# Kernel optimization log

Hardware: AMD Instinct MI355X
Metric: run time of the kernel (lower is better)

Reference implementation:

```python
import jax, jax.numpy as jnp
import numpy as np
import math

N, DIN, H, D = 3072, 512, 16, 64
HD = H * D


def mish(x):
    return x * jnp.tanh(jax.nn.softplus(x))


def setup_inputs() -> dict:
    key = jax.random.key(0)
    ks = jax.random.split(key, 10)
    s_in = 1.0 / math.sqrt(DIN)
    s_hd = 1.0 / math.sqrt(HD)
    return {
        "q": jax.random.normal(ks[0], (N, DIN), jnp.float32),
        "k": jax.random.normal(ks[1], (N, DIN), jnp.float32),
        "v": jax.random.normal(ks[2], (N, DIN), jnp.float32),
        "bias": jax.random.normal(ks[3], (N, N), jnp.float32),
        "mask": jax.random.randint(ks[4], (N, N), 0, 2, jnp.int32),
        # q/k/v projections (xavier-like init, zero bias as in _reset_parameters)
        "Wq": jax.random.normal(ks[5], (HD, DIN), jnp.float32) * s_in,
        "bq": jnp.zeros((HD,), jnp.float32),
        "Wk": jax.random.normal(ks[6], (HD, DIN), jnp.float32) * s_in,
        "bk": jnp.zeros((HD,), jnp.float32),
        "Wv": jax.random.normal(ks[7], (HD, DIN), jnp.float32) * s_in,
        "bv": jnp.zeros((HD,), jnp.float32),
        # o_proj = Linear(HD,HD) -> Mish -> Linear(HD,DIN)
        "Wo1": jax.random.normal(ks[8], (HD, HD), jnp.float32) * s_hd,
        "bo1": jnp.zeros((HD,), jnp.float32),
        "Wo2": jax.random.normal(ks[9], (DIN, HD), jnp.float32) * s_hd,
        "bo2": jnp.zeros((DIN,), jnp.float32),
    }


def reference(q, k, v, bias, mask, Wq, bq, Wk, bk, Wv, bv, Wo1, bo1, Wo2, bo2):
    # forward(..., embed_bias=True, embed_value=True) path
    n = q.shape[0]
    # project and split heads: [N, DIN] -> [H, N, D]
    qh = (q @ Wq.T + bq).reshape(n, H, D).transpose(1, 0, 2)
    kh = (k @ Wk.T + bk).reshape(n, H, D).transpose(1, 0, 2)
    vh = (v @ Wv.T + bv).reshape(n, H, D).transpose(1, 0, 2)
    # scaled dot product with additive bias (broadcast over heads) + mask fill
    logits = jnp.einsum('hnd,hmd->hnm', qh, kh) / math.sqrt(D)
    logits = logits + bias[None, :, :]
    logits = jnp.where(mask[None, :, :] == 0, jnp.float32(-9e15), logits)
    attn = jax.nn.softmax(logits, axis=-1)           # [H, N, N]
    vals = jnp.einsum('hnm,hmd->hnd', attn, vh)      # [H, N, D]
    vals = vals.transpose(1, 0, 2).reshape(n, HD)    # [N, H*D]
    # o_proj MLP (dropout = 0)
    out = mish(vals @ Wo1.T + bo1) @ Wo2.T + bo2     # [N, DIN]
    return (out, bias)
```

## Files before the change

kernel.cpp:

```cpp
#include <hip/hip_runtime.h>
#include <hip/hip_bf16.h>

#define NT 3072
#define DIN_ 512
#define NH 16
#define DH 64
#define HDIM 1024

typedef unsigned short u16;
typedef unsigned int u32;
typedef short short8 __attribute__((ext_vector_type(8)));
typedef float f32x4 __attribute__((ext_vector_type(4)));
typedef __bf16 bf16x8 __attribute__((ext_vector_type(8)));

__device__ __forceinline__ u16 f2bf(float f){
  union { float f; unsigned u; } v; v.f = f;
  unsigned r = v.u + 0x7fffu + ((v.u >> 16) & 1u);
  return (u16)(r >> 16);
}
__device__ __forceinline__ float bf2f(u16 b){
  union { unsigned u; float f; } v; v.u = ((unsigned)b) << 16;
  return v.f;
}

__global__ __launch_bounds__(256) void prep_k(
    const float* __restrict__ bias, const int* __restrict__ mask,
    u16* __restrict__ bm, float* __restrict__ bias_out)
{
  int i = blockIdx.x * 256 + threadIdx.x;
  f32x4 b = ((const f32x4*)bias)[i];
  int4 m = ((const int4*)mask)[i];
  ((f32x4*)bias_out)[i] = b;
  const int mm[4] = {m.x, m.y, m.z, m.w};
  union { u16 s[4]; unsigned long long ll; } pk;
  #pragma unroll
  for (int j = 0; j < 4; ++j)
    pk.s[j] = mm[j] ? f2bf(b[j]) : f2bf(-1e30f);
  ((unsigned long long*)bm)[i] = pk.ll;
}

__global__ __launch_bounds__(256) void cvtw_k(
    const float* __restrict__ Wq, const float* __restrict__ Wk,
    const float* __restrict__ Wv, const float* __restrict__ Wo1,
    const float* __restrict__ Wo2,
    u16* __restrict__ wqb, u16* __restrict__ wkb, u16* __restrict__ wvb,
    u16* __restrict__ wo1b, u16* __restrict__ wo2b)
{
  const float* src; u16* dst; int n4;
  switch (blockIdx.y) {
    case 0: src = Wq;  dst = wqb;  n4 = HDIM*DIN_/4; break;
    case 1: src = Wk;  dst = wkb;  n4 = HDIM*DIN_/4; break;
    case 2: src = Wv;  dst = wvb;  n4 = HDIM*DIN_/4; break;
    case 3: src = Wo1; dst = wo1b; n4 = HDIM*HDIM/4; break;
    default: src = Wo2; dst = wo2b; n4 = DIN_*HDIM/4; break;
  }
  int i = blockIdx.x * 256 + threadIdx.x;
  if (i >= n4) return;
  f32x4 v = ((const f32x4*)src)[i];
  ushort4 o;
  o.x = f2bf(v[0]); o.y = f2bf(v[1]); o.z = f2bf(v[2]); o.w = f2bf(v[3]);
  ((ushort4*)dst)[i] = o;
}

template<int A_BF16, int EPI>
__device__ __forceinline__ void gemm_body(
    const void* __restrict__ Aptr, const u16* __restrict__ W,
    const float* __restrict__ bvec, void* __restrict__ Cptr,
    int Nc, int K, float scale, int bm0, int bn0,
    u16* As, u16* Bs)
{
  const int tid = threadIdx.x;
  const int lane = tid & 63;
  const int wid = tid >> 6;
  const int wr = wid >> 1, wc = wid & 1;
  const int g = lane >> 4, lr = lane & 15;

  f32x4 acc[4][4] = {};

  for (int k0 = 0; k0 < K; k0 += 32) {
    __syncthreads();
    if (A_BF16) {
      const u16* A = (const u16*)Aptr;
      #pragma unroll
      for (int it = 0; it < 2; ++it) {
        int e = it*2048 + tid*8;
        int r = e >> 5, kk = e & 31;
        *(short8*)&As[r*40 + kk] = *(const short8*)&A[(size_t)(bm0+r)*K + k0 + kk];
      }
    } else {
      const float* A = (const float*)Aptr;
      #pragma unroll
      for (int it = 0; it < 4; ++it) {
        int e = it*1024 + tid*4;
        int r = e >> 5, kk = e & 31;
        f32x4 v = *(const f32x4*)&A[(size_t)(bm0+r)*K + k0 + kk];
        union { u16 s[4]; unsigned long long ll; } pk;
        #pragma unroll
        for (int jj = 0; jj < 4; ++jj) pk.s[jj] = f2bf(v[jj]);
        *(unsigned long long*)&As[r*40 + kk] = pk.ll;
      }
    }
    {
      #pragma unroll
      for (int it = 0; it < 2; ++it) {
        int e = it*2048 + tid*8;
        int r = e >> 5, kk = e & 31;
        *(short8*)&Bs[r*40 + kk] = *(const short8*)&W[(size_t)(bn0+r)*K + k0 + kk];
      }
    }
    __syncthreads();
    bf16x8 af[4], bfr[4];
    #pragma unroll
    for (int m = 0; m < 4; ++m)
      af[m] = *(const bf16x8*)&As[(wr*64 + m*16 + lr)*40 + g*8];
    #pragma unroll
    for (int n = 0; n < 4; ++n)
      bfr[n] = *(const bf16x8*)&Bs[(wc*64 + n*16 + lr)*40 + g*8];
    #pragma unroll
    for (int m = 0; m < 4; ++m)
      #pragma unroll
      for (int n = 0; n < 4; ++n)
        acc[m][n] = __builtin_amdgcn_mfma_f32_16x16x32_bf16(af[m], bfr[n], acc[m][n], 0, 0, 0);
  }

  #pragma unroll
  for (int m = 0; m < 4; ++m) {
    const int row0 = bm0 + wr*64 + m*16 + g*4;
    #pragma unroll
    for (int n = 0; n < 4; ++n) {
      const int col = bn0 + wc*64 + n*16 + lr;
      const float bb = bvec[col];
      #pragma unroll
      for (int j = 0; j < 4; ++j) {
        float x = acc[m][n][j] + bb;
        if (EPI == 0) x *= scale;
        if (EPI == 1) {
          float sp = (x > 15.f) ? x : log1pf(__expf(x));
          x = x * tanhf(sp);
        }
        if (EPI == 2)
          ((float*)Cptr)[(size_t)(row0+j)*Nc + col] = x;
        else
          ((u16*)Cptr)[(size_t)(row0+j)*Nc + col] = f2bf(x);
      }
    }
  }
}

template<int A_BF16, int EPI>
__global__ __launch_bounds__(256) void gemm_k(
    const void* __restrict__ Aptr, const u16* __restrict__ W,
    const float* __restrict__ bvec, void* __restrict__ Cptr,
    int Nc, int K, float scale)
{
  __shared__ __align__(16) u16 As[128*40];
  __shared__ __align__(16) u16 Bs[128*40];
  gemm_body<A_BF16, EPI>(Aptr, W, bvec, Cptr, Nc, K, scale,
                         blockIdx.x*128, blockIdx.y*128, As, Bs);
}

__global__ __launch_bounds__(256) void qkv_k(
    const float* __restrict__ q, const float* __restrict__ k,
    const float* __restrict__ v,
    const u16* __restrict__ wqb, const float* __restrict__ bq,
    const u16* __restrict__ wkb, const float* __restrict__ bk,
    const u16* __restrict__ wvb, const float* __restrict__ bv,
    u16* __restrict__ qh, u16* __restrict__ kh, u16* __restrict__ vh)
{
  __shared__ __align__(16) u16 As[128*40];
  __shared__ __align__(16) u16 Bs[128*40];
  const int sel = blockIdx.y >> 3;
  const float* A    = sel == 0 ? q   : (sel == 1 ? k   : v);
  const u16* W      = sel == 0 ? wqb : (sel == 1 ? wkb : wvb);
  const float* bvec = sel == 0 ? bq  : (sel == 1 ? bk  : bv);
  u16* C            = sel == 0 ? qh  : (sel == 1 ? kh  : vh);
  const float scale = sel == 0 ? 0.125f : 1.0f;
  gemm_body<0, 0>(A, W, bvec, C, HDIM, DIN_, scale,
                  blockIdx.x*128, (blockIdx.y & 7)*128, As, Bs);
}

__global__ __launch_bounds__(256) void attn_k(
    const u16* __restrict__ qh, const u16* __restrict__ kh,
    const u16* __restrict__ vh, const u16* __restrict__ bm,
    u16* __restrict__ vals)
{
  __shared__ __align__(16) u16 Qs[64*72];
  __shared__ __align__(16) u16 Ks[64*72];
  __shared__ __align__(16) u16 Vts[64*72];
  __shared__ __align__(16) u16 Ps[4][16*72];

  const int tid = threadIdx.x;
  const int lane = tid & 63;
  const int w = tid >> 6;
  const int g = lane >> 4, lr = lane & 15;
  const int i0 = blockIdx.x * 64;
  const int hoff = blockIdx.y * DH;

  #pragma unroll
  for (int it = 0; it < 2; ++it) {
    int c = it*256 + tid;
    int r = c >> 3, co = (c & 7) * 8;
    *(short8*)&Qs[r*72 + co] = *(const short8*)&qh[(size_t)(i0 + r)*HDIM + hoff + co];
  }
  __syncthreads();
  bf16x8 qf[2];
  #pragma unroll
  for (int kc = 0; kc < 2; ++kc)
    qf[kc] = *(const bf16x8*)&Qs[(w*16 + lr)*72 + kc*32 + g*8];

  f32x4 Oa[4] = {};
  float mr = -1e30f, ls = 0.f;
  const size_t bmrow = (size_t)(i0 + w*16 + lr) * NT;

  for (int j = 0; j < NT/64; ++j) {
    const int c0 = j * 64;
    __syncthreads();
    #pragma unroll
    for (int it = 0; it < 2; ++it) {
      int c = it*256 + tid;
      int r = c >> 3, co = (c & 7) * 8;
      *(short8*)&Ks[r*72 + co] = *(const short8*)&kh[(size_t)(c0 + r)*HDIM + hoff + co];
    }
    #pragma unroll
    for (int it = 0; it < 2; ++it) {
      int c = it*256 + tid;
      int vr = c >> 3, dco = (c & 7) * 8;
      short8 vv = *(const short8*)&vh[(size_t)(c0 + vr)*HDIM + hoff + dco];
      #pragma unroll
      for (int jj = 0; jj < 8; ++jj) {
        int d = dco + jj;
        int byte = d*144 + vr*2;
        byte ^= ((d >> 3) & 7) << 4;
        *(u16*)((char*)Vts + byte) = (u16)vv[jj];
      }
    }
    __syncthreads();

    f32x4 Sa[4];
    #pragma unroll
    for (int n = 0; n < 4; ++n) {
      ushort4 bb = *(const ushort4*)&bm[bmrow + c0 + n*16 + g*4];
      Sa[n][0] = bf2f(bb.x); Sa[n][1] = bf2f(bb.y);
      Sa[n][2] = bf2f(bb.z); Sa[n][3] = bf2f(bb.w);
    }
    #pragma unroll
    for (int kc = 0; kc < 2; ++kc)
      #pragma unroll
      for (int n = 0; n < 4; ++n) {
        bf16x8 kb = *(const bf16x8*)&Ks[(n*16 + lr)*72 + kc*32 + g*8];
        Sa[n] = __builtin_amdgcn_mfma_f32_16x16x32_bf16(kb, qf[kc], Sa[n], 0, 0, 0);
      }

    float tmax = -1e30f;
    #pragma unroll
    for (int n = 0; n < 4; ++n)
      #pragma unroll
      for (int jr = 0; jr < 4; ++jr)
        tmax = fmaxf(tmax, Sa[n][jr]);
    tmax = fmaxf(tmax, __shfl_xor(tmax, 16, 64));
    tmax = fmaxf(tmax, __shfl_xor(tmax, 32, 64));
    float mnew = fmaxf(mr, tmax);
    float alpha_me = __expf(mr - mnew);
    mr = mnew;
    float ps = 0.f;
    #pragma unroll
    for (int n = 0; n < 4; ++n)
      #pragma unroll
      for (int jr = 0; jr < 4; ++jr) {
        float p = __expf(Sa[n][jr] - mnew);
        Sa[n][jr] = p;
        ps += p;
      }
    ps += __shfl_xor(ps, 16, 64);
    ps += __shfl_xor(ps, 32, 64);
    ls = ls * alpha_me + ps;

    float av[4];
    #pragma unroll
    for (int jr = 0; jr < 4; ++jr)
      av[jr] = __shfl(alpha_me, g*4 + jr, 16);
    #pragma unroll
    for (int n = 0; n < 4; ++n)
      #pragma unroll
      for (int jr = 0; jr < 4; ++jr)
        Oa[n][jr] *= av[jr];

    #pragma unroll
    for (int n = 0; n < 4; ++n) {
      ushort4 pk;
      pk.x = f2bf(Sa[n][0]); pk.y = f2bf(Sa[n][1]);
      pk.z = f2bf(Sa[n][2]); pk.w = f2bf(Sa[n][3]);
      *(ushort4*)&Ps[w][lr*72 + n*16 + g*4] = pk;
    }
    __asm__ volatile("s_waitcnt lgkmcnt(0)" ::: "memory");
    __builtin_amdgcn_sched_barrier(0);

    #pragma unroll
    for (int kc = 0; kc < 2; ++kc) {
      bf16x8 pa = *(const bf16x8*)&Ps[w][lr*72 + kc*32 + g*8];
      #pragma unroll
      for (int n = 0; n < 4; ++n) {
        int d = n*16 + lr;
        int byte = d*144 + (kc*32 + g*8)*2;
        byte ^= ((d >> 3) & 7) << 4;
        bf16x8 vb = *(const bf16x8*)((const char*)Vts + byte);
        Oa[n] = __builtin_amdgcn_mfma_f32_16x16x32_bf16(pa, vb, Oa[n], 0, 0, 0);
      }
    }
  }

  float lv[4];
  #pragma unroll
  for (int jr = 0; jr < 4; ++jr)
    lv[jr] = 1.f / __shfl(ls, g*4 + jr, 16);
  #pragma unroll
  for (int n = 0; n < 4; ++n) {
    #pragma unroll
    for (int jr = 0; jr < 4; ++jr) {
      float o = Oa[n][jr] * lv[jr];
      int row = i0 + w*16 + g*4 + jr;
      vals[(size_t)row*HDIM + hoff + n*16 + lr] = f2bf(o);
    }
  }
}

extern "C" void kernel_launch(void* const* d_in, const int* in_sizes, int n_in,
                              void* d_out, int out_size, void* d_ws, size_t ws_size,
                              hipStream_t stream) {
  const float* q    = (const float*)d_in[0];
  const float* k    = (const float*)d_in[1];
  const float* v    = (const float*)d_in[2];
  const float* bias = (const float*)d_in[3];
  const int*   mask = (const int*)d_in[4];
  const float* Wq   = (const float*)d_in[5];
  const float* bq   = (const float*)d_in[6];
  const float* Wk   = (const float*)d_in[7];
  const float* bk   = (const float*)d_in[8];
  const float* Wv   = (const float*)d_in[9];
  const float* bv   = (const float*)d_in[10];
  const float* Wo1  = (const float*)d_in[11];
  const float* bo1  = (const float*)d_in[12];
  const float* Wo2  = (const float*)d_in[13];
  const float* bo2  = (const float*)d_in[14];

  float* out = (float*)d_out;
  float* bias_out = out + (size_t)NT * DIN_;

  char* ws = (char*)d_ws;
  u16* bm    = (u16*)ws; ws += (size_t)NT*NT*2;
  u16* qh    = (u16*)ws; ws += (size_t)NT*HDIM*2;
  u16* kh    = (u16*)ws; ws += (size_t)NT*HDIM*2;
  u16* vh    = (u16*)ws; ws += (size_t)NT*HDIM*2;
  u16* vals  = (u16*)ws; ws += (size_t)NT*HDIM*2;
  u16* wqb   = (u16*)ws; ws += (size_t)HDIM*DIN_*2;
  u16* wkb   = (u16*)ws; ws += (size_t)HDIM*DIN_*2;
  u16* wvb   = (u16*)ws; ws += (size_t)HDIM*DIN_*2;
  u16* wo1b  = (u16*)ws; ws += (size_t)HDIM*HDIM*2;
  u16* wo2b  = (u16*)ws; ws += (size_t)DIN_*HDIM*2;
  u16* t1    = qh;

  cvtw_k<<<dim3(1024, 5), 256, 0, stream>>>(Wq, Wk, Wv, Wo1, Wo2,
                                            wqb, wkb, wvb, wo1b, wo2b);
  prep_k<<<dim3(NT*NT/4/256), 256, 0, stream>>>(bias, mask, bm, bias_out);

  qkv_k<<<dim3(NT/128, 24), 256, 0, stream>>>(q, k, v, wqb, bq, wkb, bk, wvb, bv,
                                              qh, kh, vh);

  attn_k<<<dim3(NT/64, NH), 256, 0, stream>>>(qh, kh, vh, bm, vals);

  gemm_k<1,1><<<dim3(NT/128, HDIM/128), 256, 0, stream>>>(vals, wo1b, bo1, t1, HDIM, HDIM, 1.0f);
  gemm_k<1,2><<<dim3(NT/128, DIN_/128), 256, 0, stream>>>(t1, wo2b, bo2, out, DIN_, HDIM, 1.0f);
}
```

Baseline: 418.1 us.

## Write V transposed from projection GEMM and XOR-swizzle attention LDS tiles

The V projection epilogue now writes V already transposed ([HD, N] layout), so the attention kernel loads V^T tiles with vectorized 16-byte copies instead of scattering 8 scalar u16 stores per thread into LDS. K, V^T and P tiles in shared memory switch from padded 72-element rows to unpadded 64-element rows with an XOR swizzle, to avoid bank conflicts and shrink LDS use. The transposed epilogue writes ushort4 with a stride of NT, which may coalesce less well in the QKV GEMM.

```diff
diff --git a/kernel.cpp b/kernel.cpp
--- a/kernel.cpp
+++ b/kernel.cpp
@@ -21,6 +21,13 @@
 __device__ __forceinline__ float bf2f(u16 b){
   union { unsigned u; float f; } v; v.u = ((unsigned)b) << 16;
   return v.f;
+}
+
+__device__ __forceinline__ char* swz(void* base, int row, int colbyte){
+  return (char*)base + row*128 + (colbyte ^ ((row & 7) << 4));
+}
+__device__ __forceinline__ const char* swz(const void* base, int row, int colbyte){
+  return (const char*)base + row*128 + (colbyte ^ ((row & 7) << 4));
 }
 
 __global__ __launch_bounds__(256) void prep_k(
@@ -130,18 +137,27 @@
     for (int n = 0; n < 4; ++n) {
       const int col = bn0 + wc*64 + n*16 + lr;
       const float bb = bvec[col];
-      #pragma unroll
-      for (int j = 0; j < 4; ++j) {
-        float x = acc[m][n][j] + bb;
-        if (EPI == 0) x *= scale;
-        if (EPI == 1) {
-          float sp = (x > 15.f) ? x : log1pf(__expf(x));
-          x = x * tanhf(sp);
+      if (EPI == 3) {
+        ushort4 pk;
+        pk.x = f2bf((acc[m][n][0] + bb) * scale);
+        pk.y = f2bf((acc[m][n][1] + bb) * scale);
+        pk.z = f2bf((acc[m][n][2] + bb) * scale);
+        pk.w = f2bf((acc[m][n][3] + bb) * scale);
+        *(ushort4*)&((u16*)Cptr)[(size_t)col*NT + row0] = pk;
+      } else {
+        #pragma unroll
+        for (int j = 0; j < 4; ++j) {
+          float x = acc[m][n][j] + bb;
+          if (EPI == 0) x *= scale;
+          if (EPI == 1) {
+            float sp = (x > 15.f) ? x : log1pf(__expf(x));
+            x = x * tanhf(sp);
+          }
+          if (EPI == 2)
+            ((float*)Cptr)[(size_t)(row0+j)*Nc + col] = x;
+          else
+            ((u16*)Cptr)[(size_t)(row0+j)*Nc + col] = f2bf(x);
         }
-        if (EPI == 2)
-          ((float*)Cptr)[(size_t)(row0+j)*Nc + col] = x;
-        else
-          ((u16*)Cptr)[(size_t)(row0+j)*Nc + col] = f2bf(x);
       }
     }
   }
@@ -165,29 +181,34 @@
     const u16* __restrict__ wqb, const float* __restrict__ bq,
     const u16* __restrict__ wkb, const float* __restrict__ bk,
     const u16* __restrict__ wvb, const float* __restrict__ bv,
-    u16* __restrict__ qh, u16* __restrict__ kh, u16* __restrict__ vh)
+    u16* __restrict__ qh, u16* __restrict__ kh, u16* __restrict__ vt)
 {
   __shared__ __align__(16) u16 As[128*40];
   __shared__ __align__(16) u16 Bs[128*40];
   const int sel = blockIdx.y >> 3;
-  const float* A    = sel == 0 ? q   : (sel == 1 ? k   : v);
-  const u16* W      = sel == 0 ? wqb : (sel == 1 ? wkb : wvb);
-  const float* bvec = sel == 0 ? bq  : (sel == 1 ? bk  : bv);
-  u16* C            = sel == 0 ? qh  : (sel == 1 ? kh  : vh);
-  const float scale = sel == 0 ? 0.125f : 1.0f;
-  gemm_body<0, 0>(A, W, bvec, C, HDIM, DIN_, scale,
-                  blockIdx.x*128, (blockIdx.y & 7)*128, As, Bs);
+  if (sel == 2) {
+    gemm_body<0, 3>(v, wvb, bv, vt, HDIM, DIN_, 1.0f,
+                    blockIdx.x*128, (blockIdx.y & 7)*128, As, Bs);
+  } else {
+    const float* A    = sel == 0 ? q   : k;
+    const u16* W      = sel == 0 ? wqb : wkb;
+    const float* bvec = sel == 0 ? bq  : bk;
+    u16* C            = sel == 0 ? qh  : kh;
+    const float scale = sel == 0 ? 0.125f : 1.0f;
+    gemm_body<0, 0>(A, W, bvec, C, HDIM, DIN_, scale,
+                    blockIdx.x*128, (blockIdx.y & 7)*128, As, Bs);
+  }
 }
 
 __global__ __launch_bounds__(256) void attn_k(
     const u16* __restrict__ qh, const u16* __restrict__ kh,
-    const u16* __restrict__ vh, const u16* __restrict__ bm,
+    const u16* __restrict__ vt, const u16* __restrict__ bm,
     u16* __restrict__ vals)
 {
   __shared__ __align__(16) u16 Qs[64*72];
-  __shared__ __align__(16) u16 Ks[64*72];
-  __shared__ __align__(16) u16 Vts[64*72];
-  __shared__ __align__(16) u16 Ps[4][16*72];
+  __shared__ __align__(16) u16 Ks[64*64];
+  __shared__ __align__(16) u16 Vts[64*64];
+  __shared__ __align__(16) u16 PsB[4][16*64];
 
   const int tid = threadIdx.x;
   const int lane = tid & 63;
@@ -208,6 +229,8 @@
   for (int kc = 0; kc < 2; ++kc)
     qf[kc] = *(const bf16x8*)&Qs[(w*16 + lr)*72 + kc*32 + g*8];
 
+  u16* Psw = &PsB[w][0];
+
   f32x4 Oa[4] = {};
   float mr = -1e30f, ls = 0.f;
   const size_t bmrow = (size_t)(i0 + w*16 + lr) * NT;
@@ -219,20 +242,13 @@
     for (int it = 0; it < 2; ++it) {
       int c = it*256 + tid;
       int r = c >> 3, co = (c & 7) * 8;
-      *(short8*)&Ks[r*72 + co] = *(const short8*)&kh[(size_t)(c0 + r)*HDIM + hoff + co];
+      *(short8*)swz(Ks, r, co*2) = *(const short8*)&kh[(size_t)(c0 + r)*HDIM + hoff + co];
     }
     #pragma unroll
     for (int it = 0; it < 2; ++it) {
       int c = it*256 + tid;
-      int vr = c >> 3, dco = (c & 7) * 8;
-      short8 vv = *(const short8*)&vh[(size_t)(c0 + vr)*HDIM + hoff + dco];
-      #pragma unroll
-      for (int jj = 0; jj < 8; ++jj) {
-        int d = dco + jj;
-        int byte = d*144 + vr*2;
-        byte ^= ((d >> 3) & 7) << 4;
-        *(u16*)((char*)Vts + byte) = (u16)vv[jj];
-      }
+      int r = c >> 3, co = (c & 7) * 8;
+      *(short8*)swz(Vts, r, co*2) = *(const short8*)&vt[(size_t)(hoff + r)*NT + c0 + co];
     }
     __syncthreads();
 
@@ -247,7 +263,7 @@
     for (int kc = 0; kc < 2; ++kc)
       #pragma unroll
       for (int n = 0; n < 4; ++n) {
-        bf16x8 kb = *(const bf16x8*)&Ks[(n*16 + lr)*72 + kc*32 + g*8];
+        bf16x8 kb = *(const bf16x8*)swz(Ks, n*16 + lr, (kc*32 + g*8)*2);
         Sa[n] = __builtin_amdgcn_mfma_f32_16x16x32_bf16(kb, qf[kc], Sa[n], 0, 0, 0);
       }
 
@@ -290,20 +306,17 @@
       ushort4 pk;
       pk.x = f2bf(Sa[n][0]); pk.y = f2bf(Sa[n][1]);
       pk.z = f2bf(Sa[n][2]); pk.w = f2bf(Sa[n][3]);
-      *(ushort4*)&Ps[w][lr*72 + n*16 + g*4] = pk;
+      *(ushort4*)swz(Psw, lr, (n*16 + g*4)*2) = pk;
     }
     __asm__ volatile("s_waitcnt lgkmcnt(0)" ::: "memory");
     __builtin_amdgcn_sched_barrier(0);
 
     #pragma unroll
     for (int kc = 0; kc < 2; ++kc) {
-      bf16x8 pa = *(const bf16x8*)&Ps[w][lr*72 + kc*32 + g*8];
+      bf16x8 pa = *(const bf16x8*)swz(Psw, lr, (kc*32 + g*8)*2);
       #pragma unroll
       for (int n = 0; n < 4; ++n) {
-        int d = n*16 + lr;
-        int byte = d*144 + (kc*32 + g*8)*2;
-        byte ^= ((d >> 3) & 7) << 4;
-        bf16x8 vb = *(const bf16x8*)((const char*)Vts + byte);
+        bf16x8 vb = *(const bf16x8*)swz(Vts, n*16 + lr, (kc*32 + g*8)*2);
         Oa[n] = __builtin_amdgcn_mfma_f32_16x16x32_bf16(pa, vb, Oa[n], 0, 0, 0);
       }
     }
@@ -350,7 +363,7 @@
   u16* bm    = (u16*)ws; ws += (size_t)NT*NT*2;
   u16* qh    = (u16*)ws; ws += (size_t)NT*HDIM*2;
   u16* kh    = (u16*)ws; ws += (size_t)NT*HDIM*2;
-  u16* vh    = (u16*)ws; ws += (size_t)NT*HDIM*2;
+  u16* vt    = (u16*)ws; ws += (size_t)HDIM*NT*2;
   u16* vals  = (u16*)ws; ws += (size_t)NT*HDIM*2;
   u16* wqb   = (u16*)ws; ws += (size_t)HDIM*DIN_*2;
   u16* wkb   = (u16*)ws; ws += (size_t)HDIM*DIN_*2;
@@ -364,9 +377,9 @@
   prep_k<<<dim3(NT*NT/4/256), 256, 0, stream>>>(bias, mask, bm, bias_out);
 
   qkv_k<<<dim3(NT/128, 24), 256, 0, stream>>>(q, k, v, wqb, bq, wkb, bk, wvb, bv,
-                                              qh, kh, vh);
-
-  attn_k<<<dim3(NT/64, NH), 256, 0, stream>>>(qh, kh, vh, bm, vals);
+                                              qh, kh, vt);
+
+  attn_k<<<dim3(NT/64, NH), 256, 0, stream>>>(qh, kh, vt, bm, vals);
 
   gemm_k<1,1><<<dim3(NT/128, HDIM/128), 256, 0, stream>>>(vals, wo1b, bo1, t1, HDIM, HDIM, 1.0f);
   gemm_k<1,2><<<dim3(NT/128, DIN_/128), 256, 0, stream>>>(t1, wo2b, bo2, out, DIN_, HDIM, 1.0f);
```

Result: no change. 411.6 us (-1.6%).
